# Performance work log

Measured on AMD Instinct MI355X. Metric: run time of the kernel, lower is better.

The kernel has to match this reference:

```python
import jax, jax.numpy as jnp
import numpy as np

PI = 3.141592653589793
TAU = 0.5          # gumbel-softmax temperature
EPS = 1e-6
B, N, D = 128, 32, 256

def _linear(x, w, b=None):
    y = x @ w.T
    return y if b is None else y + b

def _wrap(a):
    return (a + PI) % (2 * PI) - PI

def setup_inputs() -> dict:
    key = jax.random.key(0)
    ks = jax.random.split(key, 16)
    s = 0.05
    return {
        "embedding": jax.random.normal(ks[0], (B, N, 11), jnp.float32),
        "gumbel_u": jax.random.uniform(ks[1], (B * N, N - 1, 2), jnp.float32),
        "emb1_w": jax.random.normal(ks[2], (128, 5), jnp.float32) * s,
        "emb1_b": jnp.zeros((128,), jnp.float32),
        "emb2_w": jax.random.normal(ks[3], (D, 128), jnp.float32) * s,
        "emb2_b": jnp.zeros((D,), jnp.float32),
        "hm1_w": jax.random.normal(ks[4], (D, D + 7), jnp.float32) * s,
        "hm1_b": jnp.zeros((D,), jnp.float32),
        "hm2_w": jax.random.normal(ks[5], (D, D), jnp.float32) * s,
        "hm2_b": jnp.zeros((D,), jnp.float32),
        "he_w": jax.random.normal(ks[6], (2, D), jnp.float32) * s,
        "he_b": jnp.zeros((2,), jnp.float32),
        "q_w": jax.random.normal(ks[7], (D, D), jnp.float32) * s,
        "k_w": jax.random.normal(ks[8], (D, 10), jnp.float32) * s,
        "v_w": jax.random.normal(ks[9], (D, 10), jnp.float32) * s,
        "v_b": jnp.zeros((D,), jnp.float32),
        "dec_w": jax.random.normal(ks[10], (2 * D, 2 * D), jnp.float32) * s,
        "dec_b": jnp.zeros((2 * D,), jnp.float32),
    }

def reference(embedding, gumbel_u, emb1_w, emb1_b, emb2_w, emb2_b,
              hm1_w, hm1_b, hm2_w, hm2_b, he_w, he_b,
              q_w, k_w, v_w, v_b, dec_w, dec_b):
    b, n, _ = embedding.shape
    d = q_w.shape[0]
    # static off-diagonal index lists (i,j), j != i, row-major like mask indexing
    rows, cols = np.nonzero(~np.eye(n, dtype=bool))

    embed = embedding[:, :, 4:9].reshape(b * n, 5)
    position = embedding[:, :, :2]
    heading = embedding[:, :, 2:4]
    action = embedding[:, :, 7:9]
    goal = embedding[:, :, -2:]

    # agent embedding MLP (leaky_relu slope 0.01, torch default)
    h = jax.nn.leaky_relu(_linear(embed, emb1_w, emb1_b))
    agent_embed = jax.nn.leaky_relu(_linear(h, emb2_w, emb2_b)).reshape(b, n, d)

    # pairwise geometry  [b,i,j,...]
    rel_vec = position[:, None, :, :] - position[:, :, None, :]   # pos_j - pos_i
    dx, dy = rel_vec[..., 0], rel_vec[..., 1]
    rel_dist = jnp.linalg.norm(rel_vec, axis=-1, keepdims=True) / 12.0
    heading_angle_i = jnp.arctan2(heading[..., 1], heading[..., 0])[:, :, None]  # [b,n,1]
    angle = _wrap(jnp.arctan2(dy, dx) - heading_angle_i)
    hj_cos = jnp.broadcast_to(heading[:, None, :, 0], (b, n, n))
    hj_sin = jnp.broadcast_to(heading[:, None, :, 1], (b, n, n))
    action_j = jnp.broadcast_to(action[:, None, :, :], (b, n, n, 2))
    edge_features = jnp.concatenate([
        rel_dist, jnp.cos(angle)[..., None], jnp.sin(angle)[..., None],
        hj_cos[..., None], hj_sin[..., None], action_j], axis=-1)  # [b,n,n,7]

    # hard attention branch (off-diagonal pairs only)
    h_i_flat = jnp.broadcast_to(agent_embed[:, :, None, :], (b, n, n - 1, d)).reshape(b * n, n - 1, d)
    edge_flat = edge_features[:, rows, cols].reshape(b * n, n - 1, 7)
    hard_input = jnp.concatenate([h_i_flat, edge_flat], axis=-1)
    h_hard = _linear(jax.nn.relu(_linear(hard_input, hm1_w, hm1_b)), hm2_w, hm2_b)
    hard_logits = _linear(h_hard, he_w, he_b)                      # [b*n, n-1, 2]
    g = -jnp.log(-jnp.log(gumbel_u + 1e-10) + 1e-10)
    hard_soft = jax.nn.softmax((hard_logits + g) / TAU, axis=-1)
    hard_weights = hard_soft[..., 1].reshape(b, n, n - 1)

    unnorm = jnp.linalg.norm(rel_vec, axis=-1, keepdims=True)      # [b,n,n,1]
    unnorm_rel_dist = unnorm[:, rows, cols].reshape(b * n, n - 1, 1)

    # goal polar features
    goal_rel_vec = goal[:, None, :, :] - position[:, :, None, :]   # [b,n,n,2]
    goal_rel_dist = jnp.linalg.norm(goal_rel_vec, axis=-1, keepdims=True)
    goal_rel_angle = _wrap(jnp.arctan2(goal_rel_vec[..., 1], goal_rel_vec[..., 0]) - heading_angle_i)
    goal_polar = jnp.concatenate([goal_rel_dist, jnp.cos(goal_rel_angle)[..., None],
                                  jnp.sin(goal_rel_angle)[..., None]], axis=-1)
    soft_edge = jnp.concatenate([edge_features, goal_polar], axis=-1)  # [b,n,n,10]

    # soft attention (vectorized over agents; off-diagonal gather)
    q = agent_embed @ q_w.T                                         # [b,n,d]
    k = soft_edge @ k_w.T                                           # [b,n,n,d]
    v = jax.nn.relu(_linear(soft_edge, v_w, v_b))                   # [b,n,n,d]
    k_off = k[:, rows, cols].reshape(b, n, n - 1, d)
    v_off = v[:, rows, cols].reshape(b, n, n - 1, d)
    score = jnp.einsum('bnd,bnjd->bnj', q, k_off) / jnp.sqrt(jnp.float32(d))
    soft_w = jax.nn.softmax(score, axis=-1)
    combined = soft_w * hard_weights                                # [b,n,n-1]
    x = jnp.einsum('bnjd,bnj->bnd', v_off, combined).reshape(b * n, d)

    final_input = jnp.concatenate([agent_embed.reshape(b * n, d), x], axis=-1)
    output = _linear(final_input, dec_w, dec_b)                     # [b*n, 2d]

    cwn = combined / (combined.sum(axis=-1, keepdims=True) + EPS)
    mean_entropy = (-(cwn * jnp.log(cwn + EPS)).sum(axis=-1)).mean()
    comb_w = combined.reshape(n, -1)  # matches torch.stack(dim=1).reshape(n, -1)

    return (output, hard_logits[..., 1], unnorm_rel_dist, mean_entropy, hard_weights, comb_w)
```

## Files before the change

kernel.cpp:

```cpp
#include <hip/hip_runtime.h>
#include <hip/hip_bf16.h>
#include <math.h>

typedef __hip_bfloat16 bf16;
typedef short bf16x8 __attribute__((ext_vector_type(8)));
typedef float f32x4 __attribute__((ext_vector_type(4)));
typedef unsigned short u16;

#define R_TOT 4096
#define NJ 31

#define OFF_AE   0
#define OFF_QK   1048576
#define OFF_S1   2097152
#define OFF_ENT  4542464
#define OFF_X    4546560
#define OFF_W    5595136
#define W_E1W   0
#define W_E1B   640
#define W_E2P   768
#define W_E2B   33536
#define W_H1B   101120
#define W_VWP   101376
#define W_W1EP  167684
#define W_HE2P  171780
#define W_CB    173828
#define W_S1P   200452
#define W_VW    235780
#define W_VB    238340
#define W_DECWT 238596
#define W_DECB  500740
#define W_QKM   501252

#define OUT0 0
#define OUT1 2097152
#define OUT2 2224128
#define OUT3 2351104
#define OUT4 2351105
#define OUT5 2478081

__device__ __forceinline__ float b2f(bf16 x) { return __bfloat162float(x); }
__device__ __forceinline__ float ldin(const void* p, int i, int flag) {
    return flag ? b2f(((const bf16*)p)[i]) : ((const float*)p)[i];
}
__device__ __forceinline__ void stout(void* p, int i, float v, int flag) {
    if (flag) ((bf16*)p)[i] = __float2bfloat16(v);
    else      ((float*)p)[i] = v;
}
__device__ __forceinline__ u16 f2bbits(float v) {
    bf16 h = __float2bfloat16(v);
    return *(u16*)&h;
}
__device__ __forceinline__ int detect_flag(const void* emb) {
    float x = ((const float*)emb)[threadIdx.x & 63];
    int sane = (x == x) && (fabsf(x) < 1e20f);
    unsigned long long m = __ballot(sane);
    return (__popcll(m) == 64) ? 0 : 1;
}

__global__ __launch_bounds__(256) void k_prep(
        const void* emb,
        const void* e1w, const void* e1b, const void* e2w, const void* e2b,
        const void* h1w, const void* h1b, const void* qw,  const void* kw,
        const void* vw,  const void* vb,  const void* decb,
        float* W) {
    int flag = detect_flag(emb);
    int blk = blockIdx.x;
    int tid = threadIdx.x;
    if (blk < 384) {
        int p; const void* src; int ldm, Wdst;
        if (blk < 128) { p = blk * 256 + tid;         src = e2w; ldm = 128; Wdst = W_E2P; }
        else           { p = (blk - 128) * 256 + tid; src = h1w; ldm = 263; Wdst = W_S1P; }
        int jj   = p & 7;
        int lane = (p >> 3) & 63;
        int tile = p >> 9;
        int nt = tile & 15, kt = tile >> 4;
        int n = nt * 16 + (lane & 15);
        int k = kt * 32 + ((lane >> 4) << 3) + jj;
        ((u16*)(W + Wdst))[p] = f2bbits(ldin(src, n * ldm + k, flag));
    } else if (blk < 640) {
        int p = (blk - 384) * 16 + (tid >> 4);
        int l = tid & 15;
        int jj = p & 7, lane = (p >> 3) & 63, kt = p >> 9;
        int k = kt * 32 + ((lane >> 4) << 3) + jj;
        int n = lane & 15;
        float v = 0.f;
        if (n < 10) {
#pragma unroll
            for (int dd = 0; dd < 16; dd++) {
                int d = l + 16 * dd;
                v += ldin(qw, d * 256 + k, flag) * ldin(kw, d * 10 + n, flag);
            }
        }
        v += __shfl_xor(v, 1, 64); v += __shfl_xor(v, 2, 64);
        v += __shfl_xor(v, 4, 64); v += __shfl_xor(v, 8, 64);
        if (l == 0) ((u16*)(W + W_QKM))[p] = f2bbits(v);
    } else {
        int q2 = (blk - 640) * 256 + tid;
        if      (q2 < 640)   W[W_E1W  + q2]           = ldin(e1w,  q2,          flag);
        else if (q2 < 768)   W[W_E1B  + (q2 - 640)]   = ldin(e1b,  q2 - 640,    flag);
        else if (q2 < 1024)  W[W_E2B  + (q2 - 768)]   = ldin(e2b,  q2 - 768,    flag);
        else if (q2 < 1280)  W[W_H1B  + (q2 - 1024)]  = ldin(h1b,  q2 - 1024,   flag);
        else if (q2 < 3840)  W[W_VW   + (q2 - 1280)]  = ldin(vw,   q2 - 1280,   flag);
        else if (q2 < 4096)  W[W_VB   + (q2 - 3840)]  = ldin(vb,   q2 - 3840,   flag);
        else if (q2 < 4608)  W[W_DECB + (q2 - 4096)]  = ldin(decb, q2 - 4096,   flag);
    }
}

__global__ __launch_bounds__(256) void k_embed(const void* emb, const float* W_,
                                               const void* h1w, const void* h2w, const void* h2b,
                                               const void* hew, const void* heb, const void* decw,
                                               const void* vw,
                                               u16* aeb, float* qkws, float* s1ws) {
    int flag = detect_flag(emb);
    float* W = (float*)W_;
    int blk = blockIdx.x;
    int tid = threadIdx.x;
    if (blk >= 256) {
        if (blk < 1280) {
            int idx = (blk - 256) * 256 + tid;
            int jj   = idx & 7;
            int lane = (idx >> 3) & 63;
            int tile = idx >> 9;
            int nt = tile & 31, kt = tile >> 5;
            int n = nt * 16 + (lane & 15);
            int k = kt * 32 + ((lane >> 4) << 3) + jj;
            ((u16*)(W + W_DECWT))[idx] = f2bbits(ldin(decw, n * 512 + k, flag));
        } else if (blk < 1312) {
            int p = (blk - 1280) * 256 + tid;
            int jj = p & 7, lane = (p >> 3) & 63, nt = p >> 9;
            int n = nt * 16 + (lane & 15);
            int k = ((lane >> 4) << 3) + jj;
            float v = (k < 7) ? ldin(h1w, n * 263 + 256 + k, flag) : 0.f;
            ((u16*)(W + W_W1EP))[p] = f2bbits(v);
        } else if (blk < 1568) {
            int q = (blk - 1312) * 16 + (tid >> 4);
            int l = tid & 15;
            int jj = q & 7, lane = (q >> 3) & 63, kt = q >> 9;
            int n = lane & 15;
            int c = kt * 32 + ((lane >> 4) << 3) + jj;
            float v = 0.f;
            if (n < 2) {
#pragma unroll
                for (int dd = 0; dd < 16; dd++) {
                    int d = l + 16 * dd;
                    v += ldin(hew, n * 256 + d, flag) * ldin(h2w, d * 256 + c, flag);
                }
            }
            v += __shfl_xor(v, 1, 64); v += __shfl_xor(v, 2, 64);
            v += __shfl_xor(v, 4, 64); v += __shfl_xor(v, 8, 64);
            if (l == 0) ((u16*)(W + W_HE2P))[q] = f2bbits(v);
        } else if (blk == 1568) {
            if (tid < 32) {
                int i = tid >> 4, l = tid & 15;
                float v = 0.f;
#pragma unroll
                for (int dd = 0; dd < 16; dd++) {
                    int d = l + 16 * dd;
                    v += ldin(hew, i * 256 + d, flag) * ldin(h2b, d, flag);
                }
                v += __shfl_xor(v, 1, 64); v += __shfl_xor(v, 2, 64);
                v += __shfl_xor(v, 4, 64); v += __shfl_xor(v, 8, 64);
                if (l == 0) W[W_CB + i] = v + ldin(heb, i, flag);
            }
        } else {
            int p = (blk - 1569) * 256 + tid;
            int jj = p & 7, lane = (p >> 3) & 63, nt = p >> 9;
            int n = nt * 16 + (lane & 15);
            int k = ((lane >> 4) << 3) + jj;
            float v = (k < 10) ? ldin(vw, n * 10 + k, flag) : 0.f;
            ((u16*)(W + W_VWP))[p] = f2bbits(v);
        }
        return;
    }
    int r0 = blk * 16;
    __shared__ float embL[16][12];
    __shared__ u16 hB[16][136];
    __shared__ u16 aeB[16][264];
    for (int idx = tid; idx < 16 * 11; idx += 256) {
        int s = idx / 11, t = idx % 11;
        embL[s][t] = ldin(emb, (r0 + s) * 11 + t, flag);
    }
    __syncthreads();
    for (int idx = tid; idx < 16 * 128; idx += 256) {
        int s = idx >> 7, jo = idx & 127;
        float v = W[W_E1B + jo];
#pragma unroll
        for (int t = 0; t < 5; t++) v += W[W_E1W + jo * 5 + t] * embL[s][4 + t];
        hB[s][jo] = f2bbits(v > 0.f ? v : 0.01f * v);
    }
    __syncthreads();
    int wv = tid >> 6, ln = tid & 63;
    int lr = ln & 15, quad = ln >> 4;
    {
        const bf16x8* Bp = (const bf16x8*)(W + W_E2P);
        f32x4 acc[4];
#pragma unroll
        for (int nt = 0; nt < 4; nt++) acc[nt] = (f32x4){0.f, 0.f, 0.f, 0.f};
#pragma unroll
        for (int kt = 0; kt < 4; kt++) {
            bf16x8 af = *(const bf16x8*)&hB[lr][kt * 32 + (quad << 3)];
#pragma unroll
            for (int nt = 0; nt < 4; nt++) {
                bf16x8 bfr = Bp[(kt * 16 + (wv * 4 + nt)) * 64 + ln];
                acc[nt] = __builtin_amdgcn_mfma_f32_16x16x32_bf16(af, bfr, acc[nt], 0, 0, 0);
            }
        }
#pragma unroll
        for (int nt = 0; nt < 4; nt++) {
            int d = wv * 64 + nt * 16 + lr;
            float bias = W[W_E2B + d];
#pragma unroll
            for (int reg = 0; reg < 4; reg++) {
                int m = quad * 4 + reg;
                float v = acc[nt][reg] + bias;
                v = v > 0.f ? v : 0.01f * v;
                u16 bits = f2bbits(v);
                aeB[m][d] = bits;
                aeb[(r0 + m) * 256 + d] = bits;
            }
        }
    }
    __syncthreads();
    {
        const bf16x8* Bs = (const bf16x8*)(W + W_S1P);
        f32x4 sac[4];
#pragma unroll
        for (int nt = 0; nt < 4; nt++) sac[nt] = (f32x4){0.f, 0.f, 0.f, 0.f};
#pragma unroll
        for (int kt = 0; kt < 8; kt++) {
            bf16x8 af = *(const bf16x8*)&aeB[lr][kt * 32 + (quad << 3)];
#pragma unroll
            for (int nt = 0; nt < 4; nt++) {
                bf16x8 bs = Bs[(kt * 16 + (wv * 4 + nt)) * 64 + ln];
                sac[nt] = __builtin_amdgcn_mfma_f32_16x16x32_bf16(af, bs, sac[nt], 0, 0, 0);
            }
        }
#pragma unroll
        for (int nt = 0; nt < 4; nt++) {
            int d = wv * 64 + nt * 16 + lr;
            float bias = W[W_H1B + d];
#pragma unroll
            for (int reg = 0; reg < 4; reg++) {
                int m = quad * 4 + reg;
                s1ws[(r0 + m) * 256 + d] = sac[nt][reg] + bias;
            }
        }
        if (wv == 0) {
            const bf16x8* Bm = (const bf16x8*)(W + W_QKM);
            f32x4 qk = (f32x4){0.f, 0.f, 0.f, 0.f};
#pragma unroll
            for (int kt = 0; kt < 8; kt++) {
                bf16x8 af = *(const bf16x8*)&aeB[lr][kt * 32 + (quad << 3)];
                qk = __builtin_amdgcn_mfma_f32_16x16x32_bf16(af, Bm[kt * 64 + ln], qk, 0, 0, 0);
            }
            if (lr < 10) {
#pragma unroll
                for (int reg = 0; reg < 4; reg++) {
                    int m = quad * 4 + reg;
                    qkws[(r0 + m) * 10 + lr] = qk[reg];
                }
            }
        }
    }
}

__global__ __launch_bounds__(256) void k_fused(const void* emb, const void* gum,
                                               const float* s1ws, const float* qkws, const float* W,
                                               u16* xb, float* entws, void* out) {
    int flag = detect_flag(emb);
    int r = blockIdx.x;
    int b = r >> 5, i = r & 31;
    __shared__ float embB[32][12];
    __shared__ float seL[32][10];
    __shared__ u16 eA[32][40];
    __shared__ u16 a1[32][264];
    __shared__ float pj[4][32][2];
    __shared__ float cL[32];
    __shared__ float qkL[10];
    int tid = threadIdx.x;
    for (int idx = tid; idx < 32 * 11; idx += 256) {
        int s = idx / 11, t = idx % 11;
        embB[s][t] = ldin(emb, (b * 32 + s) * 11 + t, flag);
    }
    for (int idx = tid; idx < 32 * 40; idx += 256) ((u16*)eA)[idx] = 0;
    if (tid >= 64 && tid < 74) qkL[tid - 64] = qkws[r * 10 + (tid - 64)];
    __syncthreads();
    if (tid < NJ) {
        int jp = tid;
        int j = jp + (jp >= i ? 1 : 0);
        float pix = embB[i][0], piy = embB[i][1], hix = embB[i][2], hiy = embB[i][3];
        float pjx = embB[j][0], pjy = embB[j][1], hjx = embB[j][2], hjy = embB[j][3];
        float ajx = embB[j][7], ajy = embB[j][8];
        float gjx = embB[j][9], gjy = embB[j][10];
        float hn2 = hix * hix + hiy * hiy;
        float csh, snh;
        if (hn2 == 0.f) { csh = 1.f; snh = 0.f; }
        else { float invh = rsqrtf(hn2); csh = hix * invh; snh = hiy * invh; }
        float dx = pjx - pix, dy = pjy - piy;
        float d2 = dx * dx + dy * dy;
        float dist, csd, snd;
        if (d2 == 0.f) { dist = 0.f; csd = 1.f; snd = 0.f; }
        else { float invd = rsqrtf(d2); dist = d2 * invd; csd = dx * invd; snd = dy * invd; }
        float gx = gjx - pix, gy = gjy - piy;
        float g2 = gx * gx + gy * gy;
        float gdist, csg, sng;
        if (g2 == 0.f) { gdist = 0.f; csg = 1.f; sng = 0.f; }
        else { float invg = rsqrtf(g2); gdist = g2 * invg; csg = gx * invg; sng = gy * invg; }
        float f[10];
        f[0] = dist * (1.f / 12.f);
        f[1] = csd * csh + snd * snh;
        f[2] = snd * csh - csd * snh;
        f[3] = hjx; f[4] = hjy; f[5] = ajx; f[6] = ajy;
        f[7] = gdist;
        f[8] = csg * csh + sng * snh;
        f[9] = sng * csh - csg * snh;
#pragma unroll
        for (int t = 0; t < 10; t++) { seL[jp][t] = f[t]; eA[jp][t] = f2bbits(f[t]); }
        stout(out, OUT2 + r * NJ + jp, dist, flag);
    }
    __syncthreads();
    int wv = tid >> 6, ln = tid & 63;
    int lr = ln & 15, quad = ln >> 4;
    bf16x8 af0 = *(const bf16x8*)&eA[lr][quad << 3];
    bf16x8 af1 = *(const bf16x8*)&eA[16 + lr][quad << 3];
    f32x4 vacc[2][4];
    {
        const bf16x8* Bp = (const bf16x8*)(W + W_W1EP);
        const bf16x8* Bv = (const bf16x8*)(W + W_VWP);
#pragma unroll
        for (int nt = 0; nt < 4; nt++) {
            int gnt = wv * 4 + nt;
            int d = gnt * 16 + lr;
            float s1v = s1ws[r * 256 + d];
            f32x4 acc0 = (f32x4){s1v, s1v, s1v, s1v};
            f32x4 acc1 = acc0;
            bf16x8 bb = Bp[gnt * 64 + ln];
            acc0 = __builtin_amdgcn_mfma_f32_16x16x32_bf16(af0, bb, acc0, 0, 0, 0);
            acc1 = __builtin_amdgcn_mfma_f32_16x16x32_bf16(af1, bb, acc1, 0, 0, 0);
#pragma unroll
            for (int reg = 0; reg < 4; reg++) {
                a1[(quad << 2) + reg][d]      = f2bbits(fmaxf(acc0[reg], 0.f));
                a1[16 + (quad << 2) + reg][d] = f2bbits(fmaxf(acc1[reg], 0.f));
            }
            bf16x8 bv = Bv[gnt * 64 + ln];
            f32x4 z = (f32x4){0.f, 0.f, 0.f, 0.f};
            vacc[0][nt] = __builtin_amdgcn_mfma_f32_16x16x32_bf16(af0, bv, z, 0, 0, 0);
            vacc[1][nt] = __builtin_amdgcn_mfma_f32_16x16x32_bf16(af1, bv, z, 0, 0, 0);
        }
    }
    __syncthreads();
    {
        const bf16x8* Ep = (const bf16x8*)(W + W_HE2P);
        f32x4 l0 = (f32x4){0.f, 0.f, 0.f, 0.f};
        f32x4 l1 = (f32x4){0.f, 0.f, 0.f, 0.f};
#pragma unroll
        for (int kk = 0; kk < 2; kk++) {
            int kt = wv * 2 + kk;
            bf16x8 a0 = *(const bf16x8*)&a1[lr][kt * 32 + (quad << 3)];
            bf16x8 a1f = *(const bf16x8*)&a1[16 + lr][kt * 32 + (quad << 3)];
            bf16x8 bb = Ep[kt * 64 + ln];
            l0 = __builtin_amdgcn_mfma_f32_16x16x32_bf16(a0, bb, l0, 0, 0, 0);
            l1 = __builtin_amdgcn_mfma_f32_16x16x32_bf16(a1f, bb, l1, 0, 0, 0);
        }
        if (lr < 2) {
#pragma unroll
            for (int reg = 0; reg < 4; reg++) {
                pj[wv][(quad << 2) + reg][lr]      = l0[reg];
                pj[wv][16 + (quad << 2) + reg][lr] = l1[reg];
            }
        }
    }
    __syncthreads();
    if (wv == 0) {
        if (ln == 31) cL[31] = 0.f;
        float hwv = 0.f;
        if (ln < NJ) {
            float p0 = pj[0][ln][0] + pj[1][ln][0] + pj[2][ln][0] + pj[3][ln][0];
            float p1 = pj[0][ln][1] + pj[1][ln][1] + pj[2][ln][1] + pj[3][ln][1];
            float l0 = p0 + W[W_CB + 0], l1 = p1 + W[W_CB + 1];
            float u0 = ldin(gum, (r * NJ + ln) * 2 + 0, flag);
            float u1 = ldin(gum, (r * NJ + ln) * 2 + 1, flag);
            float g0 = -logf(-logf(u0 + 1e-10f) + 1e-10f);
            float g1 = -logf(-logf(u1 + 1e-10f) + 1e-10f);
            float dl = ((l1 + g1) - (l0 + g0)) * 2.0f;
            hwv = 1.f / (1.f + expf(-dl));
            stout(out, OUT1 + r * NJ + ln, l1, flag);
            stout(out, OUT4 + r * NJ + ln, hwv, flag);
        }
        float sc = -1e30f;
        if (ln < NJ) {
            float p = 0.f;
#pragma unroll
            for (int t = 0; t < 10; t++) p += qkL[t] * seL[ln][t];
            sc = p * (1.f / 16.f);
        }
        float m = sc;
#pragma unroll
        for (int s = 32; s >= 1; s >>= 1) m = fmaxf(m, __shfl_xor(m, s, 64));
        float e = (ln < NJ) ? expf(sc - m) : 0.f;
        float sum = e;
#pragma unroll
        for (int s = 32; s >= 1; s >>= 1) sum += __shfl_xor(sum, s, 64);
        float sw = e / sum;
        float cmb = sw * hwv;
        if (ln < NJ) {
            cL[ln] = cmb;
            stout(out, OUT5 + r * NJ + ln, cmb, flag);
        }
        float csum = cmb;
#pragma unroll
        for (int s = 32; s >= 1; s >>= 1) csum += __shfl_xor(csum, s, 64);
        float cwn = cmb / (csum + 1e-6f);
        float et = (ln < NJ) ? -cwn * logf(cwn + 1e-6f) : 0.f;
#pragma unroll
        for (int s = 32; s >= 1; s >>= 1) et += __shfl_xor(et, s, 64);
        if (ln == 0) entws[r] = et;
    }
    __syncthreads();
    {
        float cj[2][4];
#pragma unroll
        for (int mt = 0; mt < 2; mt++)
#pragma unroll
            for (int reg = 0; reg < 4; reg++) cj[mt][reg] = cL[mt * 16 + (quad << 2) + reg];
#pragma unroll
        for (int nt = 0; nt < 4; nt++) {
            int d = (wv * 4 + nt) * 16 + lr;
            float vb = W[W_VB + d];
            float xp = 0.f;
#pragma unroll
            for (int mt = 0; mt < 2; mt++)
#pragma unroll
                for (int reg = 0; reg < 4; reg++)
                    xp += fmaxf(vacc[mt][nt][reg] + vb, 0.f) * cj[mt][reg];
            xp += __shfl_xor(xp, 16, 64);
            xp += __shfl_xor(xp, 32, 64);
            if (quad == 0) xb[r * 256 + d] = f2bbits(xp);
        }
    }
}

__global__ __launch_bounds__(256) void k_dec(const void* emb, const u16* aeb, const u16* xb,
                                             const float* W, const float* entws, void* out) {
    int flag = detect_flag(emb);
    int r0 = (blockIdx.x >> 2) * 32;
    int nq = blockIdx.x & 3;
    __shared__ u16 finB[32][520];
    int tid = threadIdx.x;
    for (int idx = tid; idx < 32 * 512; idx += 256) {
        int s = idx >> 9, c = idx & 511;
        finB[s][c] = (c < 256) ? aeb[(r0 + s) * 256 + c] : xb[(r0 + s) * 256 + (c - 256)];
    }
    __syncthreads();
    int wv = tid >> 6, ln = tid & 63;
    int lr = ln & 15, quad = ln >> 4;
    const bf16x8* Bp = (const bf16x8*)(W + W_DECWT);
    f32x4 acc[2][2];
#pragma unroll
    for (int mt = 0; mt < 2; mt++)
#pragma unroll
        for (int nt = 0; nt < 2; nt++) acc[mt][nt] = (f32x4){0.f, 0.f, 0.f, 0.f};
#pragma unroll
    for (int kt = 0; kt < 16; kt++) {
        bf16x8 af[2];
#pragma unroll
        for (int mt = 0; mt < 2; mt++)
            af[mt] = *(const bf16x8*)&finB[mt * 16 + lr][kt * 32 + (quad << 3)];
#pragma unroll
        for (int nt = 0; nt < 2; nt++) {
            int gnt = nq * 8 + wv * 2 + nt;
            bf16x8 bfr = Bp[(kt * 32 + gnt) * 64 + ln];
#pragma unroll
            for (int mt = 0; mt < 2; mt++)
                acc[mt][nt] = __builtin_amdgcn_mfma_f32_16x16x32_bf16(af[mt], bfr, acc[mt][nt], 0, 0, 0);
        }
    }
#pragma unroll
    for (int nt = 0; nt < 2; nt++) {
        int d = (nq * 8 + wv * 2 + nt) * 16 + lr;
        float bias = W[W_DECB + d];
#pragma unroll
        for (int mt = 0; mt < 2; mt++)
#pragma unroll
            for (int reg = 0; reg < 4; reg++) {
                int m = mt * 16 + quad * 4 + reg;
                stout(out, OUT0 + (r0 + m) * 512 + d, acc[mt][nt][reg] + bias, flag);
            }
    }
    if (blockIdx.x == 0) {
        __shared__ float red[4];
        float s = 0.f;
        for (int i2 = tid; i2 < R_TOT; i2 += 256) s += entws[i2];
#pragma unroll
        for (int m = 32; m >= 1; m >>= 1) s += __shfl_xor(s, m, 64);
        if ((tid & 63) == 0) red[tid >> 6] = s;
        __syncthreads();
        if (tid == 0) {
            float t = red[0] + red[1] + red[2] + red[3];
            stout(out, OUT3, t / (float)R_TOT, flag);
        }
    }
}

extern "C" void kernel_launch(void* const* d_in, const int* in_sizes, int n_in,
                              void* d_out, int out_size, void* d_ws, size_t ws_size,
                              hipStream_t stream) {
    const void* emb  = d_in[0];
    const void* gum  = d_in[1];
    const void* e1w  = d_in[2];
    const void* e1b  = d_in[3];
    const void* e2w  = d_in[4];
    const void* e2b  = d_in[5];
    const void* h1w  = d_in[6];
    const void* h1b  = d_in[7];
    const void* h2w  = d_in[8];
    const void* h2b  = d_in[9];
    const void* hew  = d_in[10];
    const void* heb  = d_in[11];
    const void* qw   = d_in[12];
    const void* kw   = d_in[13];
    const void* vw   = d_in[14];
    const void* vb   = d_in[15];
    const void* decw = d_in[16];
    const void* decb = d_in[17];

    float* wsf = (float*)d_ws;
    u16*   aeb  = (u16*)(wsf + OFF_AE);
    float* qkws = wsf + OFF_QK;
    float* s1ws = wsf + OFF_S1;
    float* entw = wsf + OFF_ENT;
    u16*   xb   = (u16*)(wsf + OFF_X);
    float* W    = wsf + OFF_W;

    hipLaunchKernelGGL(k_prep, dim3(659), dim3(256), 0, stream,
                       emb, e1w, e1b, e2w, e2b, h1w, h1b, qw, kw, vw, vb, decb, W);
    hipLaunchKernelGGL(k_embed, dim3(1601), dim3(256), 0, stream,
                       emb, W, h1w, h2w, h2b, hew, heb, decw, vw, aeb, qkws, s1ws);
    hipLaunchKernelGGL(k_fused, dim3(4096), dim3(256), 0, stream,
                       emb, gum, s1ws, qkws, W, xb, entw, d_out);
    hipLaunchKernelGGL(k_dec, dim3(512), dim3(256), 0, stream, emb, aeb, xb, W, entw, d_out);
}
```

Measured before the change: 152.8 us.

## Split embed s1 GEMM across four blocks and process two rows per fused block

k_embed now launches four blocks per 16-row group. Each block recomputes the embedding MLP and produces one quarter of the s1 output columns, which spreads the s1 GEMM over more blocks. k_fused handles two agent rows per block instead of one, halving the grid. This amortizes the per-block setup (the embedding load and eA zeroing) and doubles the MFMA work per block, at the cost of extra registers and shared memory. The embed split adds redundant MLP computation in exchange for more parallelism.

Measured after the change: 160.9 us. +5.3%, slower.

```diff
diff --git a/kernel.cpp b/kernel.cpp
--- a/kernel.cpp
+++ b/kernel.cpp
@@ -116,9 +116,10 @@
     float* W = (float*)W_;
     int blk = blockIdx.x;
     int tid = threadIdx.x;
-    if (blk >= 256) {
-        if (blk < 1280) {
-            int idx = (blk - 256) * 256 + tid;
+    if (blk >= 1024) {
+        int t = blk - 1024;
+        if (t < 1024) {
+            int idx = t * 256 + tid;
             int jj   = idx & 7;
             int lane = (idx >> 3) & 63;
             int tile = idx >> 9;
@@ -126,15 +127,15 @@
             int n = nt * 16 + (lane & 15);
             int k = kt * 32 + ((lane >> 4) << 3) + jj;
             ((u16*)(W + W_DECWT))[idx] = f2bbits(ldin(decw, n * 512 + k, flag));
-        } else if (blk < 1312) {
-            int p = (blk - 1280) * 256 + tid;
+        } else if (t < 1056) {
+            int p = (t - 1024) * 256 + tid;
             int jj = p & 7, lane = (p >> 3) & 63, nt = p >> 9;
             int n = nt * 16 + (lane & 15);
             int k = ((lane >> 4) << 3) + jj;
             float v = (k < 7) ? ldin(h1w, n * 263 + 256 + k, flag) : 0.f;
             ((u16*)(W + W_W1EP))[p] = f2bbits(v);
-        } else if (blk < 1568) {
-            int q = (blk - 1312) * 16 + (tid >> 4);
+        } else if (t < 1312) {
+            int q = (t - 1056) * 16 + (tid >> 4);
             int l = tid & 15;
             int jj = q & 7, lane = (q >> 3) & 63, kt = q >> 9;
             int n = lane & 15;
@@ -150,7 +151,7 @@
             v += __shfl_xor(v, 1, 64); v += __shfl_xor(v, 2, 64);
             v += __shfl_xor(v, 4, 64); v += __shfl_xor(v, 8, 64);
             if (l == 0) ((u16*)(W + W_HE2P))[q] = f2bbits(v);
-        } else if (blk == 1568) {
+        } else if (t == 1312) {
             if (tid < 32) {
                 int i = tid >> 4, l = tid & 15;
                 float v = 0.f;
@@ -164,7 +165,7 @@
                 if (l == 0) W[W_CB + i] = v + ldin(heb, i, flag);
             }
         } else {
-            int p = (blk - 1569) * 256 + tid;
+            int p = (t - 1313) * 256 + tid;
             int jj = p & 7, lane = (p >> 3) & 63, nt = p >> 9;
             int n = nt * 16 + (lane & 15);
             int k = ((lane >> 4) << 3) + jj;
@@ -173,7 +174,8 @@
         }
         return;
     }
-    int r0 = blk * 16;
+    int rg = blk >> 2, nq = blk & 3;
+    int r0 = rg * 16;
     __shared__ float embL[16][12];
     __shared__ u16 hB[16][136];
     __shared__ u16 aeB[16][264];
@@ -217,36 +219,29 @@
                 v = v > 0.f ? v : 0.01f * v;
                 u16 bits = f2bbits(v);
                 aeB[m][d] = bits;
-                aeb[(r0 + m) * 256 + d] = bits;
+                if (nq == 0) aeb[(r0 + m) * 256 + d] = bits;
             }
         }
     }
     __syncthreads();
     {
         const bf16x8* Bs = (const bf16x8*)(W + W_S1P);
-        f32x4 sac[4];
-#pragma unroll
-        for (int nt = 0; nt < 4; nt++) sac[nt] = (f32x4){0.f, 0.f, 0.f, 0.f};
+        int tile = nq * 4 + wv;
+        f32x4 sac = (f32x4){0.f, 0.f, 0.f, 0.f};
 #pragma unroll
         for (int kt = 0; kt < 8; kt++) {
             bf16x8 af = *(const bf16x8*)&aeB[lr][kt * 32 + (quad << 3)];
-#pragma unroll
-            for (int nt = 0; nt < 4; nt++) {
-                bf16x8 bs = Bs[(kt * 16 + (wv * 4 + nt)) * 64 + ln];
-                sac[nt] = __builtin_amdgcn_mfma_f32_16x16x32_bf16(af, bs, sac[nt], 0, 0, 0);
-            }
-        }
-#pragma unroll
-        for (int nt = 0; nt < 4; nt++) {
-            int d = wv * 64 + nt * 16 + lr;
-            float bias = W[W_H1B + d];
-#pragma unroll
-            for (int reg = 0; reg < 4; reg++) {
-                int m = quad * 4 + reg;
-                s1ws[(r0 + m) * 256 + d] = sac[nt][reg] + bias;
-            }
-        }
-        if (wv == 0) {
+            bf16x8 bs = Bs[(kt * 16 + tile) * 64 + ln];
+            sac = __builtin_amdgcn_mfma_f32_16x16x32_bf16(af, bs, sac, 0, 0, 0);
+        }
+        int d = tile * 16 + lr;
+        float bias = W[W_H1B + d];
+#pragma unroll
+        for (int reg = 0; reg < 4; reg++) {
+            int m = quad * 4 + reg;
+            s1ws[(r0 + m) * 256 + d] = sac[reg] + bias;
+        }
+        if (nq == 0 && wv == 0) {
             const bf16x8* Bm = (const bf16x8*)(W + W_QKM);
             f32x4 qk = (f32x4){0.f, 0.f, 0.f, 0.f};
 #pragma unroll
@@ -269,25 +264,30 @@
                                                const float* s1ws, const float* qkws, const float* W,
                                                u16* xb, float* entws, void* out) {
     int flag = detect_flag(emb);
-    int r = blockIdx.x;
-    int b = r >> 5, i = r & 31;
+    int rA = blockIdx.x * 2, rB = rA + 1;
+    int b = rA >> 5, i0 = rA & 31;
     __shared__ float embB[32][12];
-    __shared__ float seL[32][10];
-    __shared__ u16 eA[32][40];
-    __shared__ u16 a1[32][264];
-    __shared__ float pj[4][32][2];
-    __shared__ float cL[32];
-    __shared__ float qkL[10];
+    __shared__ float seL[2][32][10];
+    __shared__ u16 eA[64][40];
+    __shared__ u16 a1[64][264];
+    __shared__ float pj[4][64][2];
+    __shared__ float cL[2][32];
+    __shared__ float qkL[2][10];
     int tid = threadIdx.x;
     for (int idx = tid; idx < 32 * 11; idx += 256) {
         int s = idx / 11, t = idx % 11;
         embB[s][t] = ldin(emb, (b * 32 + s) * 11 + t, flag);
     }
-    for (int idx = tid; idx < 32 * 40; idx += 256) ((u16*)eA)[idx] = 0;
-    if (tid >= 64 && tid < 74) qkL[tid - 64] = qkws[r * 10 + (tid - 64)];
-    __syncthreads();
-    if (tid < NJ) {
-        int jp = tid;
+    for (int idx = tid; idx < 64 * 40; idx += 256) ((u16*)eA)[idx] = 0;
+    if (tid >= 64 && tid < 84) {
+        int t = tid - 64;
+        qkL[t / 10][t % 10] = qkws[(rA + t / 10) * 10 + (t % 10)];
+    }
+    __syncthreads();
+    if (tid < 62) {
+        int row = tid / 31, jp = tid - row * 31;
+        int i = i0 + row;
+        int r = rA + row;
         int j = jp + (jp >= i ? 1 : 0);
         float pix = embB[i][0], piy = embB[i][1], hix = embB[i][2], hiy = embB[i][3];
         float pjx = embB[j][0], pjy = embB[j][1], hjx = embB[j][2], hjy = embB[j][3];
@@ -316,15 +316,16 @@
         f[8] = csg * csh + sng * snh;
         f[9] = sng * csh - csg * snh;
 #pragma unroll
-        for (int t = 0; t < 10; t++) { seL[jp][t] = f[t]; eA[jp][t] = f2bbits(f[t]); }
+        for (int t = 0; t < 10; t++) { seL[row][jp][t] = f[t]; eA[row * 32 + jp][t] = f2bbits(f[t]); }
         stout(out, OUT2 + r * NJ + jp, dist, flag);
     }
     __syncthreads();
     int wv = tid >> 6, ln = tid & 63;
     int lr = ln & 15, quad = ln >> 4;
-    bf16x8 af0 = *(const bf16x8*)&eA[lr][quad << 3];
-    bf16x8 af1 = *(const bf16x8*)&eA[16 + lr][quad << 3];
-    f32x4 vacc[2][4];
+    bf16x8 af[4];
+#pragma unroll
+    for (int m4 = 0; m4 < 4; m4++) af[m4] = *(const bf16x8*)&eA[m4 * 16 + lr][quad << 3];
+    f32x4 vacc[4][4];
     {
         const bf16x8* Bp = (const bf16x8*)(W + W_W1EP);
         const bf16x8* Bv = (const bf16x8*)(W + W_VWP);
@@ -332,52 +333,57 @@
         for (int nt = 0; nt < 4; nt++) {
             int gnt = wv * 4 + nt;
             int d = gnt * 16 + lr;
-            float s1v = s1ws[r * 256 + d];
-            f32x4 acc0 = (f32x4){s1v, s1v, s1v, s1v};
-            f32x4 acc1 = acc0;
+            float s1A = s1ws[rA * 256 + d];
+            float s1B = s1ws[rB * 256 + d];
             bf16x8 bb = Bp[gnt * 64 + ln];
-            acc0 = __builtin_amdgcn_mfma_f32_16x16x32_bf16(af0, bb, acc0, 0, 0, 0);
-            acc1 = __builtin_amdgcn_mfma_f32_16x16x32_bf16(af1, bb, acc1, 0, 0, 0);
-#pragma unroll
-            for (int reg = 0; reg < 4; reg++) {
-                a1[(quad << 2) + reg][d]      = f2bbits(fmaxf(acc0[reg], 0.f));
-                a1[16 + (quad << 2) + reg][d] = f2bbits(fmaxf(acc1[reg], 0.f));
-            }
             bf16x8 bv = Bv[gnt * 64 + ln];
-            f32x4 z = (f32x4){0.f, 0.f, 0.f, 0.f};
-            vacc[0][nt] = __builtin_amdgcn_mfma_f32_16x16x32_bf16(af0, bv, z, 0, 0, 0);
-            vacc[1][nt] = __builtin_amdgcn_mfma_f32_16x16x32_bf16(af1, bv, z, 0, 0, 0);
+#pragma unroll
+            for (int m4 = 0; m4 < 4; m4++) {
+                float s1v = (m4 < 2) ? s1A : s1B;
+                f32x4 acc = (f32x4){s1v, s1v, s1v, s1v};
+                acc = __builtin_amdgcn_mfma_f32_16x16x32_bf16(af[m4], bb, acc, 0, 0, 0);
+#pragma unroll
+                for (int reg = 0; reg < 4; reg++)
+                    a1[m4 * 16 + (quad << 2) + reg][d] = f2bbits(fmaxf(acc[reg], 0.f));
+                f32x4 z = (f32x4){0.f, 0.f, 0.f, 0.f};
+                vacc[m4][nt] = __builtin_amdgcn_mfma_f32_16x16x32_bf16(af[m4], bv, z, 0, 0, 0);
+            }
         }
     }
     __syncthreads();
     {
         const bf16x8* Ep = (const bf16x8*)(W + W_HE2P);
-        f32x4 l0 = (f32x4){0.f, 0.f, 0.f, 0.f};
-        f32x4 l1 = (f32x4){0.f, 0.f, 0.f, 0.f};
+        f32x4 l[4];
+#pragma unroll
+        for (int m4 = 0; m4 < 4; m4++) l[m4] = (f32x4){0.f, 0.f, 0.f, 0.f};
 #pragma unroll
         for (int kk = 0; kk < 2; kk++) {
             int kt = wv * 2 + kk;
-            bf16x8 a0 = *(const bf16x8*)&a1[lr][kt * 32 + (quad << 3)];
-            bf16x8 a1f = *(const bf16x8*)&a1[16 + lr][kt * 32 + (quad << 3)];
             bf16x8 bb = Ep[kt * 64 + ln];
-            l0 = __builtin_amdgcn_mfma_f32_16x16x32_bf16(a0, bb, l0, 0, 0, 0);
-            l1 = __builtin_amdgcn_mfma_f32_16x16x32_bf16(a1f, bb, l1, 0, 0, 0);
+#pragma unroll
+            for (int m4 = 0; m4 < 4; m4++) {
+                bf16x8 a = *(const bf16x8*)&a1[m4 * 16 + lr][kt * 32 + (quad << 3)];
+                l[m4] = __builtin_amdgcn_mfma_f32_16x16x32_bf16(a, bb, l[m4], 0, 0, 0);
+            }
         }
         if (lr < 2) {
 #pragma unroll
-            for (int reg = 0; reg < 4; reg++) {
-                pj[wv][(quad << 2) + reg][lr]      = l0[reg];
-                pj[wv][16 + (quad << 2) + reg][lr] = l1[reg];
-            }
-        }
-    }
-    __syncthreads();
-    if (wv == 0) {
-        if (ln == 31) cL[31] = 0.f;
+            for (int m4 = 0; m4 < 4; m4++)
+#pragma unroll
+                for (int reg = 0; reg < 4; reg++)
+                    pj[wv][m4 * 16 + (quad << 2) + reg][lr] = l[m4][reg];
+        }
+    }
+    __syncthreads();
+    if (wv < 2) {
+        int row = wv;
+        int r = rA + row;
+        if (ln == 31) cL[row][31] = 0.f;
         float hwv = 0.f;
         if (ln < NJ) {
-            float p0 = pj[0][ln][0] + pj[1][ln][0] + pj[2][ln][0] + pj[3][ln][0];
-            float p1 = pj[0][ln][1] + pj[1][ln][1] + pj[2][ln][1] + pj[3][ln][1];
+            int mr = row * 32 + ln;
+            float p0 = pj[0][mr][0] + pj[1][mr][0] + pj[2][mr][0] + pj[3][mr][0];
+            float p1 = pj[0][mr][1] + pj[1][mr][1] + pj[2][mr][1] + pj[3][mr][1];
             float l0 = p0 + W[W_CB + 0], l1 = p1 + W[W_CB + 1];
             float u0 = ldin(gum, (r * NJ + ln) * 2 + 0, flag);
             float u1 = ldin(gum, (r * NJ + ln) * 2 + 1, flag);
@@ -392,7 +398,7 @@
         if (ln < NJ) {
             float p = 0.f;
 #pragma unroll
-            for (int t = 0; t < 10; t++) p += qkL[t] * seL[ln][t];
+            for (int t = 0; t < 10; t++) p += qkL[row][t] * seL[row][ln][t];
             sc = p * (1.f / 16.f);
         }
         float m = sc;
@@ -405,7 +411,7 @@
         float sw = e / sum;
         float cmb = sw * hwv;
         if (ln < NJ) {
-            cL[ln] = cmb;
+            cL[row][ln] = cmb;
             stout(out, OUT5 + r * NJ + ln, cmb, flag);
         }
         float csum = cmb;
@@ -419,24 +425,34 @@
     }
     __syncthreads();
     {
-        float cj[2][4];
-#pragma unroll
-        for (int mt = 0; mt < 2; mt++)
-#pragma unroll
-            for (int reg = 0; reg < 4; reg++) cj[mt][reg] = cL[mt * 16 + (quad << 2) + reg];
+        float cj[4][4];
+#pragma unroll
+        for (int m4 = 0; m4 < 4; m4++) {
+            int row = m4 >> 1;
+#pragma unroll
+            for (int reg = 0; reg < 4; reg++)
+                cj[m4][reg] = cL[row][(m4 & 1) * 16 + (quad << 2) + reg];
+        }
 #pragma unroll
         for (int nt = 0; nt < 4; nt++) {
             int d = (wv * 4 + nt) * 16 + lr;
             float vb = W[W_VB + d];
-            float xp = 0.f;
-#pragma unroll
-            for (int mt = 0; mt < 2; mt++)
-#pragma unroll
-                for (int reg = 0; reg < 4; reg++)
-                    xp += fmaxf(vacc[mt][nt][reg] + vb, 0.f) * cj[mt][reg];
-            xp += __shfl_xor(xp, 16, 64);
-            xp += __shfl_xor(xp, 32, 64);
-            if (quad == 0) xb[r * 256 + d] = f2bbits(xp);
+            float xpA = 0.f, xpB = 0.f;
+#pragma unroll
+            for (int reg = 0; reg < 4; reg++) {
+                xpA += fmaxf(vacc[0][nt][reg] + vb, 0.f) * cj[0][reg];
+                xpA += fmaxf(vacc[1][nt][reg] + vb, 0.f) * cj[1][reg];
+                xpB += fmaxf(vacc[2][nt][reg] + vb, 0.f) * cj[2][reg];
+                xpB += fmaxf(vacc[3][nt][reg] + vb, 0.f) * cj[3][reg];
+            }
+            xpA += __shfl_xor(xpA, 16, 64);
+            xpA += __shfl_xor(xpA, 32, 64);
+            xpB += __shfl_xor(xpB, 16, 64);
+            xpB += __shfl_xor(xpB, 32, 64);
+            if (quad == 0) {
+                xb[rA * 256 + d] = f2bbits(xpA);
+                xb[rB * 256 + d] = f2bbits(xpB);
+            }
         }
     }
 }
@@ -535,9 +551,9 @@
 
     hipLaunchKernelGGL(k_prep, dim3(659), dim3(256), 0, stream,
                        emb, e1w, e1b, e2w, e2b, h1w, h1b, qw, kw, vw, vb, decb, W);
-    hipLaunchKernelGGL(k_embed, dim3(1601), dim3(256), 0, stream,
+    hipLaunchKernelGGL(k_embed, dim3(2369), dim3(256), 0, stream,
                        emb, W, h1w, h2w, h2b, hew, heb, decw, vw, aeb, qkws, s1ws);
-    hipLaunchKernelGGL(k_fused, dim3(4096), dim3(256), 0, stream,
+    hipLaunchKernelGGL(k_fused, dim3(2048), dim3(256), 0, stream,
                        emb, gum, s1ws, qkws, W, xb, entw, d_out);
     hipLaunchKernelGGL(k_dec, dim3(512), dim3(256), 0, stream, emb, aeb, xb, W, entw, d_out);
 }
```
